# Kernel tuning notes

Measured on AMD Instinct MI355X. Metric: run time of the kernel, lower is better.

## Reference

```python
import jax, jax.numpy as jnp
import numpy as np

N, D, E, P, L = 50000, 128, 800000, 9, 3
EPS = 1e-5  # torch nn.LayerNorm default eps


def _layernorm(x, g, b):
    m = jnp.mean(x, axis=-1, keepdims=True)
    v = jnp.mean((x - m) ** 2, axis=-1, keepdims=True)
    return (x - m) * jax.lax.rsqrt(v + EPS) * g + b


def _pol_transform(x, M, onehot):
    # x: (N,d), M: (P,d,d), onehot: (N,P). Equivalent to bmm(x[n] @ M[pol[n]])
    # without materializing the (N,d,d) gathered map tensor.
    return jnp.einsum('nd,np,pdk->nk', x, onehot, M)


def setup_inputs() -> dict:
    key = jax.random.key(0)
    ks = jax.random.split(key, 12)
    s = 1.0 / np.sqrt(D)  # xavier-ish scale
    f32 = jnp.float32
    return {
        'x': jax.random.normal(ks[0], (N, D), f32),
        'edge_index': jax.random.randint(ks[1], (2, E), 0, N),
        'ring_polarities': jax.random.randint(ks[2], (N,), 0, P),
        'Wr': jax.random.normal(ks[3], (L, D, D), f32) * s,          # restriction weights
        'S': jax.random.normal(ks[4], (L, P, D, D), f32) * s,        # send_maps
        'dS': jax.random.normal(ks[5], (L, P, D, D), f32) * 0.01,    # delta_send
        'R': jax.random.normal(ks[6], (L, P, D, D), f32) * s,        # receive_maps
        'dR': jax.random.normal(ks[7], (L, P, D, D), f32) * 0.01,    # delta_receive
        'res_scale': jnp.full((L,), 0.92, f32),
        'W1': jax.random.normal(ks[8], (L, D, D), f32) * s,          # update Linear 1
        'b1': jnp.zeros((L, D), f32),
        'ln_g': jnp.ones((L, D), f32),                               # update LayerNorm
        'ln_b': jnp.zeros((L, D), f32),
        'W2': jax.random.normal(ks[9], (L, D, D), f32) * s,          # update Linear 2
        'b2': jnp.zeros((L, D), f32),
        'norm_g': jnp.ones((L, D), f32),                             # output LayerNorm
        'norm_b': jnp.zeros((L, D), f32),
    }


def reference(x, edge_index, ring_polarities, Wr, S, dS, R, dR, res_scale,
              W1, b1, ln_g, ln_b, W2, b2, norm_g, norm_b):
    src, tgt = edge_index[0], edge_index[1]
    pol = ring_polarities % P
    onehot = jax.nn.one_hot(pol, P, dtype=x.dtype)  # (N,P)
    # deg is accumulated over row(=src) in the original code, then used to
    # normalize the scatter over col(=tgt) -- preserved faithfully.
    deg = jax.ops.segment_sum(jnp.ones((E,), x.dtype), src, num_segments=N)
    deg_norm = (1.0 / jnp.clip(deg, 1.0))[:, None]  # (N,1)

    residual = x
    for l in range(L):
        # send transform: map depends only on src-node polarity, so apply
        # per-node then gather (algebraically identical to per-edge bmm).
        xt = _pol_transform(x, S[l] + dS[l], onehot)          # (N,D)
        msg = xt[src] @ Wr[l].T                               # (E,D) restriction per edge
        agg = jax.ops.segment_sum(msg, tgt, num_segments=N)   # index_add scatter
        # receive transform depends only on tgt polarity; linear, so it
        # commutes with the sum over incoming edges.
        out = _pol_transform(agg, R[l] + dR[l], onehot) * deg_norm
        # update MLP (dropout inactive in eval)
        h = jax.nn.relu(_layernorm(out @ W1[l].T + b1[l], ln_g[l], ln_b[l]))
        out = h @ W2[l].T + b2[l]
        out = res_scale[l] * out + x                           # in==out residual
        x = _layernorm(out, norm_g[l], norm_b[l])
    return x + residual  # stack-level residual (res_proj is None, dims match)
```

## Files before the change

### kernel.cpp

```cpp
#include <hip/hip_runtime.h>
#include <hip/hip_bf16.h>

constexpr int N_ = 50000;
constexpr int D_ = 128;
constexpr int E_ = 800000;
constexpr int P_ = 9;
constexpr int L_ = 3;
constexpr float EPS_ = 1e-5f;

constexpr int TM = 128;
constexpr int CHUNK = 4096;
constexpr int NBK = (E_ + CHUNK - 1) / CHUNK;
constexpr int NBUK = 196;
constexpr int HHALF = 256 * NBK;
constexpr int HTOT = 2 * HHALF;
constexpr int NSB = HTOT / 1024;
constexpr int MAT = L_ * P_;

typedef short bf16x8 __attribute__((ext_vector_type(8)));
typedef float f32x4 __attribute__((ext_vector_type(4)));

#define GLD16(gp, lp)                                                        \
    __builtin_amdgcn_global_load_lds(                                        \
        (const __attribute__((address_space(1))) unsigned int*)(gp),         \
        (__attribute__((address_space(3))) unsigned int*)(lp), 16, 0, 0)

__device__ inline unsigned short f2bf(float f) {
    __hip_bfloat16 h = __float2bfloat16(f);
    return *reinterpret_cast<unsigned short*>(&h);
}
__device__ inline float bflo(unsigned u) { return __uint_as_float(u << 16); }
__device__ inline float bfhi(unsigned u) { return __uint_as_float(u & 0xffff0000u); }
__device__ inline float bf2f(unsigned short h) {
    return __uint_as_float((unsigned)h << 16);
}
__device__ inline unsigned pack2bf(float a, float b) {
    return (unsigned)f2bf(a) | ((unsigned)f2bf(b) << 16);
}


__global__ __launch_bounds__(256) void setup_nk(const int* __restrict__ ring,
                                                int* __restrict__ pol,
                                                int* __restrict__ bcnt,
                                                const int* __restrict__ ei,
                                                int* __restrict__ histG) {
    __shared__ int h[P_];
    __shared__ int hT[256], hS[256];
    int blk = blockIdx.x, tid = threadIdx.x;
    if (tid < P_) h[tid] = 0;
    hT[tid] = 0;
    hS[tid] = 0;
    __syncthreads();
    int n = blk * 256 + tid;
    if (n < N_) {
        int p = ring[n] % P_;
        pol[n] = p;
        atomicAdd(&h[p], 1);
    }
    int base = blk * CHUNK;
#pragma unroll
    for (int i = 0; i < CHUNK / 256; ++i) {
        int e = base + tid + i * 256;
        if (e < E_) {
            atomicAdd(&hS[ei[e] >> 8], 1);
            atomicAdd(&hT[ei[E_ + e] >> 8], 1);
        }
    }
    __syncthreads();
    if (tid < P_ && h[tid] > 0) atomicAdd(&bcnt[tid], h[tid]);
    histG[tid * NBK + blk] = hT[tid];
    histG[HHALF + tid * NBK + blk] = hS[tid];
}


__global__ __launch_bounds__(1024) void scanH1(int* __restrict__ a,
                                               int* __restrict__ blkSum) {
    __shared__ int wsum[16];
    int tid = threadIdx.x, lane = tid & 63, wid = tid >> 6;
    int idx = blockIdx.x * 1024 + tid;
    int v = a[idx];
    int inc = v;
#pragma unroll
    for (int o = 1; o < 64; o <<= 1) {
        int t = __shfl_up(inc, o, 64);
        if (lane >= o) inc += t;
    }
    if (lane == 63) wsum[wid] = inc;
    __syncthreads();
    if (tid < 16) {
        int s = wsum[tid];
#pragma unroll
        for (int o = 1; o < 16; o <<= 1) {
            int t = __shfl_up(s, o, 64);
            if (tid >= o) s += t;
        }
        wsum[tid] = s;
    }
    __syncthreads();
    int wexcl = (wid == 0) ? 0 : wsum[wid - 1];
    a[idx] = wexcl + inc - v;
    if (tid == 1023) blkSum[blockIdx.x] = wsum[15];
}

__global__ void scanH2(const int* __restrict__ blkSum, int* __restrict__ blkOff,
                       int* __restrict__ offT, const int* __restrict__ bcnt,
                       int* __restrict__ boff, int* __restrict__ tileOff) {
    if (threadIdx.x != 0) return;
    int run = 0;
    for (int i = 0; i < NSB; ++i) {
        blkOff[i] = run;
        run += blkSum[i];
    }
    offT[N_] = E_;
    boff[0] = 0;
    tileOff[0] = 0;
    for (int p = 0; p < P_; ++p) {
        boff[p + 1] = boff[p] + bcnt[p];
        tileOff[p + 1] = tileOff[p] + (bcnt[p] + TM - 1) / TM;
    }
}

__global__ __launch_bounds__(1024) void scanH3(int* __restrict__ a,
                                               const int* __restrict__ blkOff) {
    int idx = blockIdx.x * 1024 + threadIdx.x;
    a[idx] += blkOff[blockIdx.x];
}


__global__ __launch_bounds__(256) void scatterTS(const int* __restrict__ ei,
                                                 const int* __restrict__ histG,
                                                 unsigned* __restrict__ bufT,
                                                 unsigned char* __restrict__ bufS8) {
    __shared__ int ldsT[256], ldsS[256];
    int blk = blockIdx.x, tid = threadIdx.x;
    ldsT[tid] = histG[tid * NBK + blk];
    ldsS[tid] = histG[HHALF + tid * NBK + blk] - E_;
    __syncthreads();
    int base = blk * CHUNK;
#pragma unroll
    for (int i = 0; i < CHUNK / 256; ++i) {
        int e = base + tid + i * 256;
        if (e < E_) {
            int s = ei[e], t = ei[E_ + e];
            int pT = atomicAdd(&ldsT[t >> 8], 1);
            bufT[pT] = ((unsigned)t << 16) | (unsigned)s;
            int pS = atomicAdd(&ldsS[s >> 8], 1);
            bufS8[pS] = (unsigned char)(s & 255);
        }
    }
}


__global__ __launch_bounds__(256) void finalize3(
    const unsigned* __restrict__ bufT, const unsigned char* __restrict__ bufS8,
    const int* __restrict__ histG, int* __restrict__ offT,
    unsigned short* __restrict__ eSrc, float* __restrict__ dnorm,
    const int* __restrict__ pol, const int* __restrict__ boff,
    int* __restrict__ bcur, int* __restrict__ blist) {
    __shared__ int s0[256];
    __shared__ int s1[256];
    int bb = blockIdx.x, tid = threadIdx.x;

    if (bb < NBUK) {
        int b = bb;
        int start = histG[b * NBK];
        int end = histG[(b + 1) * NBK];
        s0[tid] = 0;
        __syncthreads();
        for (int i = start + tid; i < end; i += 256)
            atomicAdd(&s0[(bufT[i] >> 16) & 255], 1);
        __syncthreads();
        if (tid < 64) {
            int b0 = 4 * tid;
            int v0 = s0[b0], v1 = s0[b0 + 1], v2 = s0[b0 + 2], v3 = s0[b0 + 3];
            int lsum = v0 + v1 + v2 + v3;
            int inc = lsum;
#pragma unroll
            for (int o = 1; o < 64; o <<= 1) {
                int t = __shfl_up(inc, o, 64);
                if (tid >= o) inc += t;
            }
            int excl = inc - lsum;
            s1[b0] = excl;
            s1[b0 + 1] = excl + v0;
            s1[b0 + 2] = excl + v0 + v1;
            s1[b0 + 3] = excl + v0 + v1 + v2;
        }
        __syncthreads();
        int node = (b << 8) + tid;
        if (node < N_) offT[node] = start + s1[tid];
        __syncthreads();
        for (int i = start + tid; i < end; i += 256) {
            unsigned pk = bufT[i];
            int pos = start + atomicAdd(&s1[(pk >> 16) & 255], 1);
            eSrc[pos] = (unsigned short)(pk & 0xFFFF);
        }
    } else if (bb < 2 * NBUK) {
        int b = bb - NBUK;
        int start = histG[HHALF + b * NBK] - E_;
        int end = histG[HHALF + (b + 1) * NBK] - E_;
        s0[tid] = 0;
        __syncthreads();
        for (int i = start + tid; i < end; i += 256) atomicAdd(&s0[bufS8[i]], 1);
        __syncthreads();
        int node = (b << 8) + tid;
        if (node < N_) {
            int dg = s0[tid];
            dnorm[node] = 1.f / (float)(dg > 1 ? dg : 1);
        }
    } else {
        int b = bb - 2 * NBUK;
        if (tid < P_) s0[tid] = 0;
        __syncthreads();
        int n = b * 256 + tid;
        int p = 0, loc = 0;
        bool act = (n < N_);
        if (act) {
            p = pol[n];
            loc = atomicAdd(&s0[p], 1);
        }
        __syncthreads();
        if (tid < P_ && s0[tid] > 0) s1[tid] = atomicAdd(&bcur[tid], s0[tid]);
        __syncthreads();
        if (act) blist[boff[p] + s1[p] + loc] = n;
    }
}


constexpr int GCONV = N_ * D_ / 4 / 256;
constexpr int GS = L_ * P_ * D_ * D_ / 256;
constexpr int GW2 = L_ * D_ * D_ / 256;
constexpr int GSPL = (MAT + 6) * 16384 / 256;
constexpr int GPREP = GCONV + 1 + GS + GW2 + GSPL;

__global__ __launch_bounds__(256) void prep_all(
    const float* __restrict__ x, unsigned short* __restrict__ xb,
    unsigned short* __restrict__ bufAb, unsigned short* __restrict__ bufBb,
    const float* __restrict__ S, const float* __restrict__ dS,
    unsigned short* __restrict__ Sb,
    const float* __restrict__ W2, unsigned short* __restrict__ W2b,
    const float* __restrict__ R, const float* __restrict__ dR,
    const float* __restrict__ W1, const float* __restrict__ Wr,
    unsigned short* __restrict__ Arh, unsigned short* __restrict__ Arl,
    unsigned short* __restrict__ W1h, unsigned short* __restrict__ W1l,
    unsigned short* __restrict__ Wrth, unsigned short* __restrict__ Wrtl) {
    int b = blockIdx.x, tid = threadIdx.x;
    if (b < GCONV) {
        int i = b * 256 + tid;
        float4 v = ((const float4*)x)[i];
        ushort4 o;
        o.x = f2bf(v.x); o.y = f2bf(v.y); o.z = f2bf(v.z); o.w = f2bf(v.w);
        ((ushort4*)xb)[i] = o;
    } else if (b < GCONV + 1) {
        if (tid < 64) {
            ((unsigned*)(xb + (size_t)N_ * D_))[tid] = 0;
            ((unsigned*)(bufAb + (size_t)N_ * D_))[tid] = 0;
            ((unsigned*)(bufBb + (size_t)N_ * D_))[tid] = 0;
        }
    } else if (b < GCONV + 1 + GS) {
        int idx = (b - GCONV - 1) * 256 + tid;
        int base = idx / (D_ * D_);
        int rem = idx % (D_ * D_);
        int c = rem / D_, d = rem % D_;
        size_t in = (size_t)base * D_ * D_ + (size_t)d * D_ + c;
        Sb[idx] = f2bf(S[in] + dS[in]);
    } else if (b < GCONV + 1 + GS + GW2) {
        int idx = (b - GCONV - 1 - GS) * 256 + tid;
        W2b[idx] = f2bf(W2[idx]);
    } else {
        constexpr int SZ1 = MAT * 16384;
        constexpr int SZ2 = SZ1 + 3 * 16384;
        int idx = (b - GCONV - 1 - GS - GW2) * 256 + tid;
        float v;
        unsigned short* oh;
        unsigned short* ol;
        int j;
        if (idx < SZ1) {
            v = R[idx] + dR[idx];
            oh = Arh; ol = Arl; j = idx;
        } else if (idx < SZ2) {
            j = idx - SZ1;
            v = W1[j];
            oh = W1h; ol = W1l;
        } else {
            j = idx - SZ2;
            int l = j >> 14, rem = j & 16383;
            int d = rem >> 7, i = rem & 127;
            v = Wr[(l << 14) + i * 128 + d];
            oh = Wrth; ol = Wrtl;
        }
        unsigned short h = f2bf(v);
        oh[j] = h;
        ol[j] = f2bf(v - bf2f(h));
    }
}


template <bool APM, bool BPM, bool OUT_SPLIT>
__global__ __launch_bounds__(256) void small_mfma(
    const unsigned short* __restrict__ Ah, const unsigned short* __restrict__ Al,
    const unsigned short* __restrict__ Bh, const unsigned short* __restrict__ Bl,
    unsigned short* __restrict__ Oh, unsigned short* __restrict__ Ol) {
    __shared__ unsigned short stg[(OUT_SPLIT ? 2 : 1) * 64 * 136];
    int tid = threadIdx.x, b = blockIdx.x;
    int mat = b >> 1, rb = b & 1;
    int l = mat / P_;
    size_t aoff = (size_t)(APM ? mat : l) * 16384 + (size_t)rb * 8192;
    size_t boff = (size_t)(BPM ? mat : l) * 16384;
    const unsigned short* ahp = Ah + aoff;
    const unsigned short* alp = Al + aoff;
    const unsigned short* bhp = Bh + boff;
    const unsigned short* blp = Bl + boff;

    int lane = tid & 63, wave = tid >> 6;
    int n = lane & 15, q = lane >> 4;
    int wr = wave * 16;

    f32x4 acc[8];
#pragma unroll
    for (int t = 0; t < 8; ++t) acc[t] = (f32x4){0.f, 0.f, 0.f, 0.f};

    int arow = (wr + n) * 128;
#pragma unroll
    for (int kc = 0; kc < 4; ++kc) {
        int ko = kc * 32 + q * 8;
        bf16x8 avh = *(const bf16x8*)(ahp + arow + ko);
        bf16x8 avl = *(const bf16x8*)(alp + arow + ko);
#pragma unroll
        for (int t = 0; t < 8; ++t) {
            int brow = (t * 16 + n) * 128;
            bf16x8 bvh = *(const bf16x8*)(bhp + brow + ko);
            bf16x8 bvl = *(const bf16x8*)(blp + brow + ko);
            acc[t] = __builtin_amdgcn_mfma_f32_16x16x32_bf16(avh, bvh, acc[t], 0, 0, 0);
            acc[t] = __builtin_amdgcn_mfma_f32_16x16x32_bf16(avh, bvl, acc[t], 0, 0, 0);
            acc[t] = __builtin_amdgcn_mfma_f32_16x16x32_bf16(avl, bvh, acc[t], 0, 0, 0);
        }
    }
#pragma unroll
    for (int t = 0; t < 8; ++t)
#pragma unroll
        for (int r = 0; r < 4; ++r) {
            int row = wr + q * 4 + r;
            float v = acc[t][r];
            unsigned short h = f2bf(v);
            stg[row * 136 + t * 16 + n] = h;
            if constexpr (OUT_SPLIT)
                stg[64 * 136 + row * 136 + t * 16 + n] = f2bf(v - bf2f(h));
        }
    __syncthreads();
    size_t obase = (size_t)mat * 16384 + (size_t)rb * 8192;
#pragma unroll
    for (int i = 0; i < 4; ++i) {
        int c = tid + i * 256;
        int r = c >> 4, off = c & 15;
        *(uint4*)(Oh + obase + r * 128 + off * 8) =
            *(const uint4*)(stg + r * 136 + off * 8);
        if constexpr (OUT_SPLIT)
            *(uint4*)(Ol + obase + r * 128 + off * 8) =
                *(const uint4*)(stg + 64 * 136 + r * 136 + off * 8);
    }
}


__device__ inline void accum_row(float* acc, uint4 r) {
    acc[0] += bflo(r.x); acc[1] += bfhi(r.x);
    acc[2] += bflo(r.y); acc[3] += bfhi(r.y);
    acc[4] += bflo(r.z); acc[5] += bfhi(r.z);
    acc[6] += bflo(r.w); acc[7] += bfhi(r.w);
}

__global__ __launch_bounds__(256) void aggregate_bf(const unsigned short* __restrict__ xt,
                                                    const int* __restrict__ offT,
                                                    const unsigned short* __restrict__ eSrc,
                                                    unsigned short* __restrict__ agg) {
    int nd = blockIdx.x * 4 + (threadIdx.x >> 6);
    if (nd >= N_) return;
    int l = threadIdx.x & 63;
    int g = l >> 4, c16 = l & 15;
    int beg = offT[nd], end = offT[nd + 1];

    float acc[8];
#pragma unroll
    for (int k = 0; k < 8; ++k) acc[k] = 0.f;

    for (int base = beg; base < end; base += 64) {
        int cnt = min(64, end - base);
        int idxv = (l < cnt) ? (int)eSrc[base + l] : 0;
        int steps = (cnt + 3) >> 2;
        int j = 0;
        for (; j + 3 < steps; j += 4) {
            int e0 = 4 * j + g, e1 = e0 + 4, e2 = e0 + 8, e3 = e0 + 12;
            int i0 = __shfl(idxv, e0, 64);
            int i1 = __shfl(idxv, e1, 64);
            int i2 = __shfl(idxv, e2, 64);
            int i3 = __shfl(idxv, e3, 64);
            int r0 = (e0 < cnt) ? i0 : N_;
            int r1 = (e1 < cnt) ? i1 : N_;
            int r2 = (e2 < cnt) ? i2 : N_;
            int r3 = (e3 < cnt) ? i3 : N_;
            uint4 v0 = ((const uint4*)(xt + (size_t)r0 * D_))[c16];
            uint4 v1 = ((const uint4*)(xt + (size_t)r1 * D_))[c16];
            uint4 v2 = ((const uint4*)(xt + (size_t)r2 * D_))[c16];
            uint4 v3 = ((const uint4*)(xt + (size_t)r3 * D_))[c16];
            accum_row(acc, v0);
            accum_row(acc, v1);
            accum_row(acc, v2);
            accum_row(acc, v3);
        }
        for (; j < steps; ++j) {
            int e0 = 4 * j + g;
            int i0 = __shfl(idxv, e0, 64);
            int r0 = (e0 < cnt) ? i0 : N_;
            uint4 v0 = ((const uint4*)(xt + (size_t)r0 * D_))[c16];
            accum_row(acc, v0);
        }
    }
#pragma unroll
    for (int k = 0; k < 8; ++k) {
        acc[k] += __shfl_xor(acc[k], 16, 64);
        acc[k] += __shfl_xor(acc[k], 32, 64);
    }
    if (g == 0) {
        uint4 o;
        o.x = (unsigned)f2bf(acc[0]) | ((unsigned)f2bf(acc[1]) << 16);
        o.y = (unsigned)f2bf(acc[2]) | ((unsigned)f2bf(acc[3]) << 16);
        o.z = (unsigned)f2bf(acc[4]) | ((unsigned)f2bf(acc[5]) << 16);
        o.w = (unsigned)f2bf(acc[6]) | ((unsigned)f2bf(acc[7]) << 16);
        ((uint4*)(agg + (size_t)nd * D_))[c16] = o;
    }
}


__device__ inline void stage_B_async(const unsigned short* __restrict__ B,
                                     unsigned short* sB, int wave, int lane) {
    int rsub = lane >> 4, cl = lane & 15;
#pragma unroll
    for (int j = 0; j < 4; ++j) {
        int seg = wave * 4 + j;
        int row = seg * 4 + rsub;
        GLD16(B + row * 128 + ((cl ^ (row & 15)) << 3), sB + seg * 512);
    }
}

#define XCH_FRAG(dst, Pl, Ph, kc)                                            \
    {                                                                        \
        unsigned a0 = __shfl(Pl[2 * (kc)], s0, 64);                          \
        unsigned b0 = __shfl(Pl[2 * (kc) + 1], s0, 64);                      \
        unsigned a1 = __shfl(Ph[2 * (kc)], s0, 64);                          \
        unsigned b1 = __shfl(Ph[2 * (kc) + 1], s0, 64);                      \
        unsigned a2 = __shfl(Pl[2 * (kc)], s1, 64);                          \
        unsigned b2 = __shfl(Pl[2 * (kc) + 1], s1, 64);                      \
        unsigned a3 = __shfl(Ph[2 * (kc)], s1, 64);                          \
        unsigned b3 = __shfl(Ph[2 * (kc) + 1], s1, 64);                      \
        union { unsigned u[4]; bf16x8 v; } fu;                               \
        fu.u[0] = hi ? b0 : a0;                                              \
        fu.u[1] = hi ? b1 : a1;                                              \
        fu.u[2] = hi ? b2 : a2;                                              \
        fu.u[3] = hi ? b3 : a3;                                              \
        dst = fu.v;                                                          \
    }


__global__ __launch_bounds__(512, 4) void gemm_xt0(
    const unsigned short* __restrict__ A, const unsigned short* __restrict__ Bw,
    unsigned short* __restrict__ OutB, const int* __restrict__ blist,
    const int* __restrict__ boff, const int* __restrict__ tileOff) {
    __shared__ unsigned short sB[128 * 128];
    int tid = threadIdx.x, b = blockIdx.x;
    if (b >= tileOff[P_]) return;
    int pp = 0;
    while (pp < P_ - 1 && b >= tileOff[pp + 1]) ++pp;
    int tb = b - tileOff[pp];
    int cnt = boff[pp + 1] - boff[pp];
    int nrows = min(TM, cnt - tb * TM);
    int rowbase = boff[pp] + tb * TM;

    int lane = tid & 63, wave = tid >> 6;
    int n = lane & 15, q = lane >> 4;
    int rr = wave * 16 + n;
    int rw = (rr < nrows) ? blist[rowbase + rr] : -1;
    size_t grow = (rw >= 0) ? (size_t)rw : (size_t)N_;

    stage_B_async(Bw + (size_t)pp * (D_ * D_), sB, wave, lane);
    bf16x8 bg[4];
#pragma unroll
    for (int kc = 0; kc < 4; ++kc)
        bg[kc] = *(const bf16x8*)(A + grow * 128 + kc * 32 + q * 8);
    __syncthreads();

    f32x4 acc[8];
#pragma unroll
    for (int t = 0; t < 8; ++t) acc[t] = (f32x4){0.f, 0.f, 0.f, 0.f};
#pragma unroll
    for (int kc = 0; kc < 4; ++kc) {
#pragma unroll
        for (int t = 0; t < 8; ++t) {
            int cs = ((((kc << 2) + q) ^ n) << 3);
            bf16x8 af = *(const bf16x8*)(sB + (t * 16 + n) * 128 + cs);
            acc[t] = __builtin_amdgcn_mfma_f32_16x16x32_bf16(af, bg[kc], acc[t], 0, 0, 0);
        }
    }
    if (rw >= 0) {
#pragma unroll
        for (int t = 0; t < 8; ++t) {
            uint2 o;
            o.x = pack2bf(acc[t][0], acc[t][1]);
            o.y = pack2bf(acc[t][2], acc[t][3]);
            *(uint2*)(OutB + (size_t)rw * 128 + t * 16 + q * 4) = o;
        }
    }
}


template <bool LAST>
__global__ __launch_bounds__(512, 4) void fused_layer(
    const unsigned short* __restrict__ agg, const unsigned short* __restrict__ DmAll,
    const unsigned short* __restrict__ W2b, const unsigned short* __restrict__ SnAll,
    const int* __restrict__ blist, const int* __restrict__ boff,
    const int* __restrict__ tileOff, const float* __restrict__ dnorm,
    const float* __restrict__ b1v, const float* __restrict__ g1v,
    const float* __restrict__ e1v, const float* __restrict__ b2v,
    const float* __restrict__ g2v, const float* __restrict__ e2v,
    const float* __restrict__ rs_ptr, const float* __restrict__ xres,
    const float* __restrict__ x0add, float* __restrict__ OutF,
    unsigned short* __restrict__ OutXt) {
    __shared__ unsigned short sB[128 * 128];

    int tid = threadIdx.x, b = blockIdx.x;
    if (b >= tileOff[P_]) return;
    int pp = 0;
    while (pp < P_ - 1 && b >= tileOff[pp + 1]) ++pp;
    int tb = b - tileOff[pp];
    int cnt = boff[pp + 1] - boff[pp];
    int nrows = min(TM, cnt - tb * TM);
    int rowbase = boff[pp] + tb * TM;

    int lane = tid & 63, wave = tid >> 6;
    int n = lane & 15, q = lane >> 4;
    int rr = wave * 16 + n;
    int rw = (rr < nrows) ? blist[rowbase + rr] : -1;
    size_t grow = (rw >= 0) ? (size_t)rw : (size_t)N_;
    int s0 = n + ((q & 1) << 5), s1 = s0 + 16;
    bool hi = q >= 2;

    stage_B_async(DmAll + (size_t)pp * (D_ * D_), sB, wave, lane);
    bf16x8 bg[4];
#pragma unroll
    for (int kc = 0; kc < 4; ++kc)
        bg[kc] = *(const bf16x8*)(agg + grow * 128 + kc * 32 + q * 8);
    float dn = (rw >= 0) ? dnorm[rw] : 1.f;
    __syncthreads();

    f32x4 acc[8];
#pragma unroll
    for (int t = 0; t < 8; ++t) acc[t] = (f32x4){0.f, 0.f, 0.f, 0.f};
#pragma unroll
    for (int kc = 0; kc < 4; ++kc) {
#pragma unroll
        for (int t = 0; t < 8; ++t) {
            int cs = ((((kc << 2) + q) ^ n) << 3);
            bf16x8 af = *(const bf16x8*)(sB + (t * 16 + n) * 128 + cs);
            acc[t] = __builtin_amdgcn_mfma_f32_16x16x32_bf16(af, bg[kc], acc[t], 0, 0, 0);
        }
    }

    unsigned Pl[8], Ph[8];
    {
        float rs1 = 0.f, rs2 = 0.f;
#pragma unroll
        for (int t = 0; t < 8; ++t) {
            float4 bb = *(const float4*)(b1v + t * 16 + q * 4);
#pragma unroll
            for (int r = 0; r < 4; ++r) {
                float v = dn * acc[t][r] + (&bb.x)[r];
                acc[t][r] = v;
                rs1 += v;
                rs2 += v * v;
            }
        }
        rs1 += __shfl_xor(rs1, 16, 64);
        rs1 += __shfl_xor(rs1, 32, 64);
        rs2 += __shfl_xor(rs2, 16, 64);
        rs2 += __shfl_xor(rs2, 32, 64);
        float mm = rs1 * (1.f / 128.f);
        float rv = rsqrtf(rs2 * (1.f / 128.f) - mm * mm + EPS_);
#pragma unroll
        for (int t = 0; t < 8; ++t) {
            float4 gg = *(const float4*)(g1v + t * 16 + q * 4);
            float4 ee = *(const float4*)(e1v + t * 16 + q * 4);
            float h0 = fmaxf((acc[t][0] - mm) * rv * gg.x + ee.x, 0.f);
            float h1 = fmaxf((acc[t][1] - mm) * rv * gg.y + ee.y, 0.f);
            float h2 = fmaxf((acc[t][2] - mm) * rv * gg.z + ee.z, 0.f);
            float h3 = fmaxf((acc[t][3] - mm) * rv * gg.w + ee.w, 0.f);
            Pl[t] = pack2bf(h0, h1);
            Ph[t] = pack2bf(h2, h3);
        }
    }

    __syncthreads();
    stage_B_async(W2b, sB, wave, lane);
    bf16x8 h2[4];
#pragma unroll
    for (int kc = 0; kc < 4; ++kc) XCH_FRAG(h2[kc], Pl, Ph, kc)
    __syncthreads();

#pragma unroll
    for (int t = 0; t < 8; ++t) acc[t] = (f32x4){0.f, 0.f, 0.f, 0.f};
#pragma unroll
    for (int kc = 0; kc < 4; ++kc) {
#pragma unroll
        for (int t = 0; t < 8; ++t) {
            int cs = ((((kc << 2) + q) ^ n) << 3);
            bf16x8 af = *(const bf16x8*)(sB + (t * 16 + n) * 128 + cs);
            acc[t] = __builtin_amdgcn_mfma_f32_16x16x32_bf16(af, h2[kc], acc[t], 0, 0, 0);
        }
    }

    float rsc = rs_ptr[0];
    float4 xrq[8];
#pragma unroll
    for (int t = 0; t < 8; ++t) {
        if (rw >= 0)
            xrq[t] = *(const float4*)(xres + (size_t)rw * 128 + t * 16 + q * 4);
        else
            xrq[t] = float4{0.f, 0.f, 0.f, 0.f};
    }
    {
        float rs1 = 0.f, rs2 = 0.f;
#pragma unroll
        for (int t = 0; t < 8; ++t) {
            float4 bb = *(const float4*)(b2v + t * 16 + q * 4);
#pragma unroll
            for (int r = 0; r < 4; ++r) {
                float v = rsc * (acc[t][r] + (&bb.x)[r]) + (&xrq[t].x)[r];
                acc[t][r] = v;
                rs1 += v;
                rs2 += v * v;
            }
        }
        rs1 += __shfl_xor(rs1, 16, 64);
        rs1 += __shfl_xor(rs1, 32, 64);
        rs2 += __shfl_xor(rs2, 16, 64);
        rs2 += __shfl_xor(rs2, 32, 64);
        float mm = rs1 * (1.f / 128.f);
        float rv = rsqrtf(rs2 * (1.f / 128.f) - mm * mm + EPS_);
        if constexpr (LAST) {
#pragma unroll
            for (int t = 0; t < 8; ++t) {
                float4 gg = *(const float4*)(g2v + t * 16 + q * 4);
                float4 ee = *(const float4*)(e2v + t * 16 + q * 4);
                if (rw >= 0) {
                    float4 xa = *(const float4*)(x0add + (size_t)rw * 128 + t * 16 + q * 4);
                    float4 o;
                    o.x = (acc[t][0] - mm) * rv * gg.x + ee.x + xa.x;
                    o.y = (acc[t][1] - mm) * rv * gg.y + ee.y + xa.y;
                    o.z = (acc[t][2] - mm) * rv * gg.z + ee.z + xa.z;
                    o.w = (acc[t][3] - mm) * rv * gg.w + ee.w + xa.w;
                    *(float4*)(OutF + (size_t)rw * 128 + t * 16 + q * 4) = o;
                }
            }
        } else {
#pragma unroll
            for (int t = 0; t < 8; ++t) {
                float4 gg = *(const float4*)(g2v + t * 16 + q * 4);
                float4 ee = *(const float4*)(e2v + t * 16 + q * 4);
                float4 o;
                o.x = (acc[t][0] - mm) * rv * gg.x + ee.x;
                o.y = (acc[t][1] - mm) * rv * gg.y + ee.y;
                o.z = (acc[t][2] - mm) * rv * gg.z + ee.z;
                o.w = (acc[t][3] - mm) * rv * gg.w + ee.w;
                xrq[t] = o;
                Pl[t] = pack2bf(o.x, o.y);
                Ph[t] = pack2bf(o.z, o.w);
            }
        }
    }

    if constexpr (!LAST) {
        __syncthreads();
        stage_B_async(SnAll + (size_t)pp * (D_ * D_), sB, wave, lane);
        bf16x8 x2[4];
#pragma unroll
        for (int kc = 0; kc < 4; ++kc) XCH_FRAG(x2[kc], Pl, Ph, kc)
        __syncthreads();

#pragma unroll
        for (int t = 0; t < 8; ++t) acc[t] = (f32x4){0.f, 0.f, 0.f, 0.f};
#pragma unroll
        for (int kc = 0; kc < 4; ++kc) {
#pragma unroll
            for (int t = 0; t < 8; ++t) {
                int cs = ((((kc << 2) + q) ^ n) << 3);
                bf16x8 af = *(const bf16x8*)(sB + (t * 16 + n) * 128 + cs);
                acc[t] = __builtin_amdgcn_mfma_f32_16x16x32_bf16(af, x2[kc], acc[t], 0, 0, 0);
            }
        }
        if (rw >= 0) {
#pragma unroll
            for (int t = 0; t < 8; ++t) {
                uint2 o;
                o.x = pack2bf(acc[t][0], acc[t][1]);
                o.y = pack2bf(acc[t][2], acc[t][3]);
                *(uint2*)(OutXt + (size_t)rw * 128 + t * 16 + q * 4) = o;
            }
#pragma unroll
            for (int t = 0; t < 8; ++t)
                *(float4*)(OutF + (size_t)rw * 128 + t * 16 + q * 4) = xrq[t];
        }
    }
}


extern "C" void kernel_launch(void* const* d_in, const int* in_sizes, int n_in,
                              void* d_out, int out_size, void* d_ws, size_t ws_size,
                              hipStream_t stream) {
    const float* x0 = (const float*)d_in[0];
    const int* ei = (const int*)d_in[1];
    const int* ring = (const int*)d_in[2];
    const float* Wr = (const float*)d_in[3];
    const float* S = (const float*)d_in[4];
    const float* dS = (const float*)d_in[5];
    const float* R = (const float*)d_in[6];
    const float* dR = (const float*)d_in[7];
    const float* rsc = (const float*)d_in[8];
    const float* W1 = (const float*)d_in[9];
    const float* b1 = (const float*)d_in[10];
    const float* lng = (const float*)d_in[11];
    const float* lnb = (const float*)d_in[12];
    const float* W2 = (const float*)d_in[13];
    const float* b2 = (const float*)d_in[14];
    const float* ng = (const float*)d_in[15];
    const float* nb = (const float*)d_in[16];
    float* out = (float*)d_out;

    char* w = (char*)d_ws;
    auto alloc = [&](size_t bytes) {
        char* p = w;
        w += (bytes + 15) & ~(size_t)15;
        return p;
    };
    unsigned short* xb = (unsigned short*)alloc((size_t)(N_ + 1) * D_ * 2);
    unsigned short* bufAb = (unsigned short*)alloc((size_t)(N_ + 1) * D_ * 2);
    unsigned short* bufBb = (unsigned short*)alloc((size_t)(N_ + 1) * D_ * 2);
    float* xbuf = (float*)alloc((size_t)N_ * D_ * 4);
    unsigned short* Sb = (unsigned short*)alloc((size_t)L_ * P_ * D_ * D_ * 2);
    unsigned short* Dmb = (unsigned short*)alloc((size_t)L_ * P_ * D_ * D_ * 2);
    unsigned short* W2b = (unsigned short*)alloc((size_t)L_ * D_ * D_ * 2);
    unsigned short* Arh = (unsigned short*)alloc((size_t)MAT * 16384 * 2);
    unsigned short* Arl = (unsigned short*)alloc((size_t)MAT * 16384 * 2);
    unsigned short* W1h = (unsigned short*)alloc((size_t)3 * 16384 * 2);
    unsigned short* W1l = (unsigned short*)alloc((size_t)3 * 16384 * 2);
    unsigned short* Wrth = (unsigned short*)alloc((size_t)3 * 16384 * 2);
    unsigned short* Wrtl = (unsigned short*)alloc((size_t)3 * 16384 * 2);
    unsigned short* T1th = (unsigned short*)alloc((size_t)MAT * 16384 * 2);
    unsigned short* T1tl = (unsigned short*)alloc((size_t)MAT * 16384 * 2);
    float* dnorm = (float*)alloc((size_t)N_ * 4);
    int* histG = (int*)alloc((size_t)HTOT * 4);
    unsigned* bufT = (unsigned*)alloc((size_t)E_ * 4);
    unsigned char* bufS8 = (unsigned char*)alloc((size_t)E_);
    unsigned short* eSrc = (unsigned short*)alloc((size_t)E_ * 2);
    int* offT = (int*)alloc((size_t)(N_ + 1) * 4);
    int* pol = (int*)alloc((size_t)N_ * 4);
    int* boff = (int*)alloc((size_t)(P_ + 1) * 4);
    int* tileOff = (int*)alloc((size_t)(P_ + 1) * 4);
    int* blist = (int*)alloc((size_t)N_ * 4);
    int* blkSum = (int*)alloc((size_t)NSB * 4);
    int* blkOff = (int*)alloc((size_t)NSB * 4);
    int* bcnt = (int*)alloc((size_t)2 * P_ * 4);
    int* bcur = bcnt + P_;

    hipMemsetAsync(bcnt, 0, (size_t)2 * P_ * 4, stream);

    const int BTILES = N_ / TM + P_;

    setup_nk<<<NBK, 256, 0, stream>>>(ring, pol, bcnt, ei, histG);
    scanH1<<<NSB, 1024, 0, stream>>>(histG, blkSum);
    scanH2<<<1, 64, 0, stream>>>(blkSum, blkOff, offT, bcnt, boff, tileOff);
    scanH3<<<NSB, 1024, 0, stream>>>(histG, blkOff);
    scatterTS<<<NBK, 256, 0, stream>>>(ei, histG, bufT, bufS8);
    finalize3<<<3 * NBUK, 256, 0, stream>>>(bufT, bufS8, histG, offT, eSrc, dnorm,
                                            pol, boff, bcur, blist);
    prep_all<<<GPREP, 256, 0, stream>>>(x0, xb, bufAb, bufBb, S, dS, Sb, W2, W2b,
                                        R, dR, W1, Wr, Arh, Arl, W1h, W1l, Wrth, Wrtl);
    small_mfma<false, true, true><<<2 * MAT, 256, 0, stream>>>(
        W1h, W1l, Arh, Arl, T1th, T1tl);
    small_mfma<true, false, false><<<2 * MAT, 256, 0, stream>>>(
        T1th, T1tl, Wrth, Wrtl, Dmb, nullptr);

    gemm_xt0<<<BTILES, 512, 0, stream>>>(xb, Sb, bufAb, blist, boff, tileOff);

    for (int l = 0; l < L_; ++l) {
        const size_t lPDD = (size_t)l * P_ * D_ * D_;
        const size_t lDD = (size_t)l * D_ * D_;
        const size_t lD = (size_t)l * D_;
        aggregate_bf<<<N_ / 4, 256, 0, stream>>>(bufAb, offT, eSrc, bufBb);
        const float* xr = (l == 0) ? x0 : xbuf;
        if (l < L_ - 1) {
            fused_layer<false><<<BTILES, 512, 0, stream>>>(
                bufBb, Dmb + lPDD, W2b + lDD, Sb + lPDD + (size_t)P_ * D_ * D_,
                blist, boff, tileOff, dnorm,
                b1 + lD, lng + lD, lnb + lD, b2 + lD, ng + lD, nb + lD,
                rsc + l, xr, nullptr, xbuf, bufAb);
        } else {
            fused_layer<true><<<BTILES, 512, 0, stream>>>(
                bufBb, Dmb + lPDD, W2b + lDD, nullptr,
                blist, boff, tileOff, dnorm,
                b1 + lD, lng + lD, lnb + lD, b2 + lD, ng + lD, nb + lD,
                rsc + l, xr, x0, out, nullptr);
        }
    }
}
```

Baseline: 363.5 us.

## Store node features in polarity-sorted order to drop row gathers

```diff
diff --git a/kernel.cpp b/kernel.cpp
--- a/kernel.cpp
+++ b/kernel.cpp
@@ -130,22 +130,48 @@
 __global__ __launch_bounds__(256) void scatterTS(const int* __restrict__ ei,
                                                  const int* __restrict__ histG,
                                                  unsigned* __restrict__ bufT,
-                                                 unsigned char* __restrict__ bufS8) {
-    __shared__ int ldsT[256], ldsS[256];
+                                                 unsigned char* __restrict__ bufS8,
+                                                 const int* __restrict__ pol,
+                                                 const int* __restrict__ boff,
+                                                 int* __restrict__ bcur,
+                                                 int* __restrict__ blist,
+                                                 int* __restrict__ perm) {
+    __shared__ int s0[256], s1[256];
     int blk = blockIdx.x, tid = threadIdx.x;
-    ldsT[tid] = histG[tid * NBK + blk];
-    ldsS[tid] = histG[HHALF + tid * NBK + blk] - E_;
-    __syncthreads();
-    int base = blk * CHUNK;
-#pragma unroll
-    for (int i = 0; i < CHUNK / 256; ++i) {
-        int e = base + tid + i * 256;
-        if (e < E_) {
-            int s = ei[e], t = ei[E_ + e];
-            int pT = atomicAdd(&ldsT[t >> 8], 1);
-            bufT[pT] = ((unsigned)t << 16) | (unsigned)s;
-            int pS = atomicAdd(&ldsS[s >> 8], 1);
-            bufS8[pS] = (unsigned char)(s & 255);
+    if (blk < NBK) {
+        s0[tid] = histG[tid * NBK + blk];
+        s1[tid] = histG[HHALF + tid * NBK + blk] - E_;
+        __syncthreads();
+        int base = blk * CHUNK;
+#pragma unroll
+        for (int i = 0; i < CHUNK / 256; ++i) {
+            int e = base + tid + i * 256;
+            if (e < E_) {
+                int s = ei[e], t = ei[E_ + e];
+                int pT = atomicAdd(&s0[t >> 8], 1);
+                bufT[pT] = ((unsigned)t << 16) | (unsigned)s;
+                int pS = atomicAdd(&s1[s >> 8], 1);
+                bufS8[pS] = (unsigned char)(s & 255);
+            }
+        }
+    } else {
+        int b = blk - NBK;
+        if (tid < P_) s0[tid] = 0;
+        __syncthreads();
+        int n = b * 256 + tid;
+        int p = 0, loc = 0;
+        bool act = (n < N_);
+        if (act) {
+            p = pol[n];
+            loc = atomicAdd(&s0[p], 1);
+        }
+        __syncthreads();
+        if (tid < P_ && s0[tid] > 0) s1[tid] = atomicAdd(&bcur[tid], s0[tid]);
+        __syncthreads();
+        if (act) {
+            int pos = boff[p] + s1[p] + loc;
+            blist[pos] = n;
+            perm[n] = pos;
         }
     }
 }
@@ -154,9 +180,8 @@
 __global__ __launch_bounds__(256) void finalize3(
     const unsigned* __restrict__ bufT, const unsigned char* __restrict__ bufS8,
     const int* __restrict__ histG, int* __restrict__ offT,
-    unsigned short* __restrict__ eSrc, float* __restrict__ dnorm,
-    const int* __restrict__ pol, const int* __restrict__ boff,
-    int* __restrict__ bcur, int* __restrict__ blist) {
+    unsigned short* __restrict__ eSrc, float* __restrict__ dnormp,
+    const int* __restrict__ perm) {
     __shared__ int s0[256];
     __shared__ int s1[256];
     int bb = blockIdx.x, tid = threadIdx.x;
@@ -193,9 +218,9 @@
         for (int i = start + tid; i < end; i += 256) {
             unsigned pk = bufT[i];
             int pos = start + atomicAdd(&s1[(pk >> 16) & 255], 1);
-            eSrc[pos] = (unsigned short)(pk & 0xFFFF);
-        }
-    } else if (bb < 2 * NBUK) {
+            eSrc[pos] = (unsigned short)perm[pk & 0xFFFF];
+        }
+    } else {
         int b = bb - NBUK;
         int start = histG[HHALF + b * NBK] - E_;
         int end = histG[HHALF + (b + 1) * NBK] - E_;
@@ -206,23 +231,8 @@
         int node = (b << 8) + tid;
         if (node < N_) {
             int dg = s0[tid];
-            dnorm[node] = 1.f / (float)(dg > 1 ? dg : 1);
-        }
-    } else {
-        int b = bb - 2 * NBUK;
-        if (tid < P_) s0[tid] = 0;
-        __syncthreads();
-        int n = b * 256 + tid;
-        int p = 0, loc = 0;
-        bool act = (n < N_);
-        if (act) {
-            p = pol[n];
-            loc = atomicAdd(&s0[p], 1);
-        }
-        __syncthreads();
-        if (tid < P_ && s0[tid] > 0) s1[tid] = atomicAdd(&bcur[tid], s0[tid]);
-        __syncthreads();
-        if (act) blist[boff[p] + s1[p] + loc] = n;
+            dnormp[perm[node]] = 1.f / (float)(dg > 1 ? dg : 1);
+        }
     }
 }
 
@@ -235,6 +245,7 @@
 
 __global__ __launch_bounds__(256) void prep_all(
     const float* __restrict__ x, unsigned short* __restrict__ xb,
+    float* __restrict__ x0p, const int* __restrict__ perm,
     unsigned short* __restrict__ bufAb, unsigned short* __restrict__ bufBb,
     const float* __restrict__ S, const float* __restrict__ dS,
     unsigned short* __restrict__ Sb,
@@ -247,10 +258,13 @@
     int b = blockIdx.x, tid = threadIdx.x;
     if (b < GCONV) {
         int i = b * 256 + tid;
+        int row = i >> 5, c = i & 31;
+        int p = perm[row];
         float4 v = ((const float4*)x)[i];
         ushort4 o;
         o.x = f2bf(v.x); o.y = f2bf(v.y); o.z = f2bf(v.z); o.w = f2bf(v.w);
-        ((ushort4*)xb)[i] = o;
+        ((ushort4*)xb)[(size_t)p * 32 + c] = o;
+        ((float4*)x0p)[(size_t)p * 32 + c] = v;
     } else if (b < GCONV + 1) {
         if (tid < 64) {
             ((unsigned*)(xb + (size_t)N_ * D_))[tid] = 0;
@@ -372,12 +386,14 @@
 __global__ __launch_bounds__(256) void aggregate_bf(const unsigned short* __restrict__ xt,
                                                     const int* __restrict__ offT,
                                                     const unsigned short* __restrict__ eSrc,
+                                                    const int* __restrict__ perm,
                                                     unsigned short* __restrict__ agg) {
     int nd = blockIdx.x * 4 + (threadIdx.x >> 6);
     if (nd >= N_) return;
     int l = threadIdx.x & 63;
     int g = l >> 4, c16 = l & 15;
     int beg = offT[nd], end = offT[nd + 1];
+    int pdst = perm[nd];
 
     float acc[8];
 #pragma unroll
@@ -426,7 +442,7 @@
         o.y = (unsigned)f2bf(acc[2]) | ((unsigned)f2bf(acc[3]) << 16);
         o.z = (unsigned)f2bf(acc[4]) | ((unsigned)f2bf(acc[5]) << 16);
         o.w = (unsigned)f2bf(acc[6]) | ((unsigned)f2bf(acc[7]) << 16);
-        ((uint4*)(agg + (size_t)nd * D_))[c16] = o;
+        ((uint4*)(agg + (size_t)pdst * D_))[c16] = o;
     }
 }
 
@@ -463,7 +479,7 @@
 
 __global__ __launch_bounds__(512, 4) void gemm_xt0(
     const unsigned short* __restrict__ A, const unsigned short* __restrict__ Bw,
-    unsigned short* __restrict__ OutB, const int* __restrict__ blist,
+    unsigned short* __restrict__ OutB,
     const int* __restrict__ boff, const int* __restrict__ tileOff) {
     __shared__ unsigned short sB[128 * 128];
     int tid = threadIdx.x, b = blockIdx.x;
@@ -478,14 +494,13 @@
     int lane = tid & 63, wave = tid >> 6;
     int n = lane & 15, q = lane >> 4;
     int rr = wave * 16 + n;
-    int rw = (rr < nrows) ? blist[rowbase + rr] : -1;
-    size_t grow = (rw >= 0) ? (size_t)rw : (size_t)N_;
+    size_t posr = (size_t)(rowbase + rr);
 
     stage_B_async(Bw + (size_t)pp * (D_ * D_), sB, wave, lane);
     bf16x8 bg[4];
 #pragma unroll
     for (int kc = 0; kc < 4; ++kc)
-        bg[kc] = *(const bf16x8*)(A + grow * 128 + kc * 32 + q * 8);
+        bg[kc] = *(const bf16x8*)(A + posr * 128 + kc * 32 + q * 8);
     __syncthreads();
 
     f32x4 acc[8];
@@ -500,13 +515,13 @@
             acc[t] = __builtin_amdgcn_mfma_f32_16x16x32_bf16(af, bg[kc], acc[t], 0, 0, 0);
         }
     }
-    if (rw >= 0) {
+    if (rr < nrows) {
 #pragma unroll
         for (int t = 0; t < 8; ++t) {
             uint2 o;
             o.x = pack2bf(acc[t][0], acc[t][1]);
             o.y = pack2bf(acc[t][2], acc[t][3]);
-            *(uint2*)(OutB + (size_t)rw * 128 + t * 16 + q * 4) = o;
+            *(uint2*)(OutB + posr * 128 + t * 16 + q * 4) = o;
         }
     }
 }
@@ -517,12 +532,12 @@
     const unsigned short* __restrict__ agg, const unsigned short* __restrict__ DmAll,
     const unsigned short* __restrict__ W2b, const unsigned short* __restrict__ SnAll,
     const int* __restrict__ blist, const int* __restrict__ boff,
-    const int* __restrict__ tileOff, const float* __restrict__ dnorm,
+    const int* __restrict__ tileOff, const float* __restrict__ dnormp,
     const float* __restrict__ b1v, const float* __restrict__ g1v,
     const float* __restrict__ e1v, const float* __restrict__ b2v,
     const float* __restrict__ g2v, const float* __restrict__ e2v,
-    const float* __restrict__ rs_ptr, const float* __restrict__ xres,
-    const float* __restrict__ x0add, float* __restrict__ OutF,
+    const float* __restrict__ rs_ptr, const float* __restrict__ xresp,
+    const float* __restrict__ x0p, float* __restrict__ OutF,
     unsigned short* __restrict__ OutXt) {
     __shared__ unsigned short sB[128 * 128];
 
@@ -538,8 +553,7 @@
     int lane = tid & 63, wave = tid >> 6;
     int n = lane & 15, q = lane >> 4;
     int rr = wave * 16 + n;
-    int rw = (rr < nrows) ? blist[rowbase + rr] : -1;
-    size_t grow = (rw >= 0) ? (size_t)rw : (size_t)N_;
+    size_t posr = (size_t)(rowbase + rr);
     int s0 = n + ((q & 1) << 5), s1 = s0 + 16;
     bool hi = q >= 2;
 
@@ -547,8 +561,8 @@
     bf16x8 bg[4];
 #pragma unroll
     for (int kc = 0; kc < 4; ++kc)
-        bg[kc] = *(const bf16x8*)(agg + grow * 128 + kc * 32 + q * 8);
-    float dn = (rw >= 0) ? dnorm[rw] : 1.f;
+        bg[kc] = *(const bf16x8*)(agg + posr * 128 + kc * 32 + q * 8);
+    float dn = dnormp[posr];
     __syncthreads();
 
     f32x4 acc[8];
@@ -619,12 +633,8 @@
     float rsc = rs_ptr[0];
     float4 xrq[8];
 #pragma unroll
-    for (int t = 0; t < 8; ++t) {
-        if (rw >= 0)
-            xrq[t] = *(const float4*)(xres + (size_t)rw * 128 + t * 16 + q * 4);
-        else
-            xrq[t] = float4{0.f, 0.f, 0.f, 0.f};
-    }
+    for (int t = 0; t < 8; ++t)
+        xrq[t] = *(const float4*)(xresp + posr * 128 + t * 16 + q * 4);
     {
         float rs1 = 0.f, rs2 = 0.f;
 #pragma unroll
@@ -645,12 +655,13 @@
         float mm = rs1 * (1.f / 128.f);
         float rv = rsqrtf(rs2 * (1.f / 128.f) - mm * mm + EPS_);
         if constexpr (LAST) {
+            int rw = (rr < nrows) ? blist[posr] : -1;
 #pragma unroll
             for (int t = 0; t < 8; ++t) {
                 float4 gg = *(const float4*)(g2v + t * 16 + q * 4);
                 float4 ee = *(const float4*)(e2v + t * 16 + q * 4);
+                float4 xa = *(const float4*)(x0p + posr * 128 + t * 16 + q * 4);
                 if (rw >= 0) {
-                    float4 xa = *(const float4*)(x0add + (size_t)rw * 128 + t * 16 + q * 4);
                     float4 o;
                     o.x = (acc[t][0] - mm) * rv * gg.x + ee.x + xa.x;
                     o.y = (acc[t][1] - mm) * rv * gg.y + ee.y + xa.y;
@@ -695,17 +706,17 @@
                 acc[t] = __builtin_amdgcn_mfma_f32_16x16x32_bf16(af, x2[kc], acc[t], 0, 0, 0);
             }
         }
-        if (rw >= 0) {
+        if (rr < nrows) {
 #pragma unroll
             for (int t = 0; t < 8; ++t) {
                 uint2 o;
                 o.x = pack2bf(acc[t][0], acc[t][1]);
                 o.y = pack2bf(acc[t][2], acc[t][3]);
-                *(uint2*)(OutXt + (size_t)rw * 128 + t * 16 + q * 4) = o;
+                *(uint2*)(OutXt + posr * 128 + t * 16 + q * 4) = o;
             }
 #pragma unroll
             for (int t = 0; t < 8; ++t)
-                *(float4*)(OutF + (size_t)rw * 128 + t * 16 + q * 4) = xrq[t];
+                *(float4*)(OutF + posr * 128 + t * 16 + q * 4) = xrq[t];
         }
     }
 }
@@ -739,10 +750,12 @@
         w += (bytes + 15) & ~(size_t)15;
         return p;
     };
-    unsigned short* xb = (unsigned short*)alloc((size_t)(N_ + 1) * D_ * 2);
-    unsigned short* bufAb = (unsigned short*)alloc((size_t)(N_ + 1) * D_ * 2);
-    unsigned short* bufBb = (unsigned short*)alloc((size_t)(N_ + 1) * D_ * 2);
-    float* xbuf = (float*)alloc((size_t)N_ * D_ * 4);
+    const size_t NP = (size_t)N_ + TM + 1;
+    unsigned short* xb = (unsigned short*)alloc(NP * D_ * 2);
+    unsigned short* bufAb = (unsigned short*)alloc(NP * D_ * 2);
+    unsigned short* bufBb = (unsigned short*)alloc(NP * D_ * 2);
+    float* xbuf = (float*)alloc(NP * D_ * 4);
+    float* x0p = (float*)alloc(NP * D_ * 4);
     unsigned short* Sb = (unsigned short*)alloc((size_t)L_ * P_ * D_ * D_ * 2);
     unsigned short* Dmb = (unsigned short*)alloc((size_t)L_ * P_ * D_ * D_ * 2);
     unsigned short* W2b = (unsigned short*)alloc((size_t)L_ * D_ * D_ * 2);
@@ -754,7 +767,7 @@
     unsigned short* Wrtl = (unsigned short*)alloc((size_t)3 * 16384 * 2);
     unsigned short* T1th = (unsigned short*)alloc((size_t)MAT * 16384 * 2);
     unsigned short* T1tl = (unsigned short*)alloc((size_t)MAT * 16384 * 2);
-    float* dnorm = (float*)alloc((size_t)N_ * 4);
+    float* dnormp = (float*)alloc(NP * 4);
     int* histG = (int*)alloc((size_t)HTOT * 4);
     unsigned* bufT = (unsigned*)alloc((size_t)E_ * 4);
     unsigned char* bufS8 = (unsigned char*)alloc((size_t)E_);
@@ -763,7 +776,8 @@
     int* pol = (int*)alloc((size_t)N_ * 4);
     int* boff = (int*)alloc((size_t)(P_ + 1) * 4);
     int* tileOff = (int*)alloc((size_t)(P_ + 1) * 4);
-    int* blist = (int*)alloc((size_t)N_ * 4);
+    int* blist = (int*)alloc(NP * 4);
+    int* perm = (int*)alloc((size_t)N_ * 4);
     int* blkSum = (int*)alloc((size_t)NSB * 4);
     int* blkOff = (int*)alloc((size_t)NSB * 4);
     int* bcnt = (int*)alloc((size_t)2 * P_ * 4);
@@ -777,36 +791,38 @@
     scanH1<<<NSB, 1024, 0, stream>>>(histG, blkSum);
     scanH2<<<1, 64, 0, stream>>>(blkSum, blkOff, offT, bcnt, boff, tileOff);
     scanH3<<<NSB, 1024, 0, stream>>>(histG, blkOff);
-    scatterTS<<<NBK, 256, 0, stream>>>(ei, histG, bufT, bufS8);
-    finalize3<<<3 * NBUK, 256, 0, stream>>>(bufT, bufS8, histG, offT, eSrc, dnorm,
-                                            pol, boff, bcur, blist);
-    prep_all<<<GPREP, 256, 0, stream>>>(x0, xb, bufAb, bufBb, S, dS, Sb, W2, W2b,
+    scatterTS<<<NBK + NBUK, 256, 0, stream>>>(ei, histG, bufT, bufS8,
+                                              pol, boff, bcur, blist, perm);
+    finalize3<<<2 * NBUK, 256, 0, stream>>>(bufT, bufS8, histG, offT, eSrc,
+                                            dnormp, perm);
+    prep_all<<<GPREP, 256, 0, stream>>>(x0, xb, x0p, perm, bufAb, bufBb,
+                                        S, dS, Sb, W2, W2b,
                                         R, dR, W1, Wr, Arh, Arl, W1h, W1l, Wrth, Wrtl);
     small_mfma<false, true, true><<<2 * MAT, 256, 0, stream>>>(
         W1h, W1l, Arh, Arl, T1th, T1tl);
     small_mfma<true, false, false><<<2 * MAT, 256, 0, stream>>>(
         T1th, T1tl, Wrth, Wrtl, Dmb, nullptr);
 
-    gemm_xt0<<<BTILES, 512, 0, stream>>>(xb, Sb, bufAb, blist, boff, tileOff);
+    gemm_xt0<<<BTILES, 512, 0, stream>>>(xb, Sb, bufAb, boff, tileOff);
 
     for (int l = 0; l < L_; ++l) {
         const size_t lPDD = (size_t)l * P_ * D_ * D_;
         const size_t lDD = (size_t)l * D_ * D_;
         const size_t lD = (size_t)l * D_;
-        aggregate_bf<<<N_ / 4, 256, 0, stream>>>(bufAb, offT, eSrc, bufBb);
-        const float* xr = (l == 0) ? x0 : xbuf;
+        aggregate_bf<<<N_ / 4, 256, 0, stream>>>(bufAb, offT, eSrc, perm, bufBb);
+        const float* xrp = (l == 0) ? x0p : xbuf;
         if (l < L_ - 1) {
             fused_layer<false><<<BTILES, 512, 0, stream>>>(
                 bufBb, Dmb + lPDD, W2b + lDD, Sb + lPDD + (size_t)P_ * D_ * D_,
-                blist, boff, tileOff, dnorm,
+                blist, boff, tileOff, dnormp,
                 b1 + lD, lng + lD, lnb + lD, b2 + lD, ng + lD, nb + lD,
-                rsc + l, xr, nullptr, xbuf, bufAb);
+                rsc + l, xrp, nullptr, xbuf, bufAb);
         } else {
             fused_layer<true><<<BTILES, 512, 0, stream>>>(
                 bufBb, Dmb + lPDD, W2b + lDD, nullptr,
-                blist, boff, tileOff, dnorm,
+                blist, boff, tileOff, dnormp,
                 b1 + lD, lng + lD, lnb + lD, b2 + lD, ng + lD, nb + lD,
-                rsc + l, xr, x0, out, nullptr);
-        }
-    }
-}
+                rsc + l, xrp, x0p, out, nullptr);
+        }
+    }
+}
```

New measurement: 372.4 us. 1.02x slower.
